# Kernel optimization log

Hardware: AMD Instinct MI355X
Metric: run time of the kernel (lower is better)

## Reference

```python
import jax, jax.numpy as jnp
import numpy as np

B, H, N, D, BD, K = 8, 8, 65536, 128, 64, 32


def _l2norm(x, eps=1e-12):
    n = jnp.linalg.norm(x, axis=-1, keepdims=True)
    return x / jnp.maximum(n, eps)


def _topk_sparse_softmax(sim, k):
    # softmax over the top-k entries per (b,h); zeros elsewhere (== masked_fill -inf softmax)
    vals, idx = jax.lax.top_k(sim, k)              # [B,H,k]
    wk = jax.nn.softmax(vals, axis=-1)
    b = jnp.arange(sim.shape[0])[:, None, None]
    h = jnp.arange(sim.shape[1])[None, :, None]
    return jnp.zeros_like(sim).at[b, h, idx].set(wk)  # [B,H,N]


def setup_inputs() -> dict:
    key = jax.random.key(0)
    ks = jax.random.split(key, 14)
    return {
        "memory": jax.random.normal(ks[0], (B, N, D), jnp.float32),
        "read_keys": jax.random.normal(ks[1], (B, H, D), jnp.float32),
        "write_keys": jax.random.normal(ks[2], (B, H, D), jnp.float32),
        "write_vals": jax.random.normal(ks[3], (B, H, D), jnp.float32),
        "erase": jax.random.uniform(ks[4], (B, H), jnp.float32),
        "add_gate": jax.random.uniform(ks[5], (B, H), jnp.float32),
        "beta_r": jax.random.uniform(ks[6], (B, H), jnp.float32),
        "beta_w": jax.random.uniform(ks[7], (B, H), jnp.float32),
        "W_b1": jax.random.normal(ks[8], (D, BD), jnp.float32) * 0.02,
        "b_b1": jnp.zeros((BD,), jnp.float32),
        "W_b2": jax.random.normal(ks[9], (BD, D), jnp.float32) * 0.02,
        "b_b2": jnp.zeros((D,), jnp.float32),
        "W_merge": jax.random.normal(ks[10], (H * D, D), jnp.float32) * 0.02,
        "b_merge": jnp.zeros((D,), jnp.float32),
        "ln_g": jnp.ones((D,), jnp.float32),
        "ln_b": jnp.zeros((D,), jnp.float32),
        "decay_gate": jnp.ones((N,), jnp.float32) * 0.99,
    }


def reference(memory, read_keys, write_keys, write_vals, erase, add_gate,
              beta_r, beta_w, W_b1, b_b1, W_b2, b_b2, W_merge, b_merge,
              ln_g, ln_b, decay_gate):
    # ---- write (erase/add with top-k addressing, head-mean, normalize, decay) ----
    cvals = jax.nn.gelu(write_vals @ W_b1 + b_b1, approximate=False) @ W_b2 + b_b2  # [B,H,D]
    sim_w = jnp.einsum('bhd,bnd->bhn', _l2norm(write_keys), _l2norm(memory)) * beta_w[..., None]
    ww = _topk_sparse_softmax(sim_w, K)                                # [B,H,N]
    # mean_h[mem*(1-w*e)] = mem*(1-mean_h(w*e));  mean_h[w*add*cvals] via einsum/H
    erase_mean = (ww * erase[..., None]).mean(axis=1)                  # [B,N]
    add_part = jnp.einsum('bhn,bhd->bnd', ww * add_gate[..., None], cvals) / H
    mem2 = memory * (1.0 - erase_mean)[..., None] + add_part
    mem2 = _l2norm(mem2 + 1e-8)
    mem2 = mem2 * jax.nn.sigmoid(decay_gate)[None, :, None]            # decay gate

    # ---- read (from updated memory) ----
    sim_r = jnp.einsum('bhd,bnd->bhn', _l2norm(read_keys), _l2norm(mem2)) * beta_r[..., None]
    wr = _topk_sparse_softmax(sim_r, K)
    rph = jnp.einsum('bhn,bnd->bhd', wr, mem2).reshape(mem2.shape[0], H * D)
    merged = rph @ W_merge + b_merge                                   # [B,D]
    mu = merged.mean(axis=-1, keepdims=True)
    var = jnp.mean((merged - mu) ** 2, axis=-1, keepdims=True)
    out = (merged - mu) / jnp.sqrt(var + 1e-5) * ln_g + ln_b           # LayerNorm
    return out
```

## Files before the change

kernel.cpp:

```cpp
#include <hip/hip_runtime.h>
#include <hip/hip_bf16.h>

#define BB   8
#define HH   8
#define NN   65536
#define DD   128
#define BDIM 64
#define KK   32


#define OFF_SIMW 0u
#define OFF_SIMR (OFF_SIMW + 4194304u)
#define OFF_NWK  (OFF_SIMR + 4194304u)
#define OFF_NRK  (OFF_NWK + 8192u)
#define OFF_CV   (OFF_NRK + 8192u)
#define OFF_WIDX (OFF_CV + 8192u)
#define OFF_WVAL (OFF_WIDX + 2048u)
#define OFF_RIDX (OFF_WVAL + 2048u)
#define OFF_RVAL (OFF_RIDX + 2048u)
#define OFF_M2U  (OFF_RVAL + 2048u)
#define OFF_RPH  (OFF_M2U + 262144u)

__device__ __forceinline__ float brsum128(float v, float* sred, int tid) {
  #pragma unroll
  for (int o = 32; o > 0; o >>= 1) v += __shfl_xor(v, o);
  __syncthreads();
  if ((tid & 63) == 0) sred[tid >> 6] = v;
  __syncthreads();
  return sred[0] + sred[1];
}

__global__ __launch_bounds__(128) void k1_setup(
    const float* __restrict__ wkeys, const float* __restrict__ rkeys,
    const float* __restrict__ wvals,
    const float* __restrict__ beta_r, const float* __restrict__ beta_w,
    const float* __restrict__ W_b1, const float* __restrict__ b_b1,
    const float* __restrict__ W_b2, const float* __restrict__ b_b2,
    float* __restrict__ nwk, float* __restrict__ nrk,
    float* __restrict__ cvals, float* __restrict__ rph) {
  int g = blockIdx.x;
  int d = threadIdx.x;
  __shared__ float sred[2];
  __shared__ float wv_s[DD];
  __shared__ float hid[BDIM];

  rph[g * DD + d] = 0.f;

  float wk = wkeys[g * DD + d];
  float rk = rkeys[g * DD + d];
  float wv = wvals[g * DD + d];
  wv_s[d] = wv;

  float s = brsum128(wk * wk, sred, d);
  nwk[g * DD + d] = wk / fmaxf(sqrtf(s), 1e-12f) * beta_w[g];
  s = brsum128(rk * rk, sred, d);
  nrk[g * DD + d] = rk / fmaxf(sqrtf(s), 1e-12f) * beta_r[g];

  __syncthreads();
  if (d < BDIM) {
    float a = b_b1[d];
    #pragma unroll 4
    for (int dd = 0; dd < DD; ++dd) a += wv_s[dd] * W_b1[dd * BDIM + d];
    hid[d] = a * 0.5f * (1.f + erff(a * 0.70710678118654752f));
  }
  __syncthreads();
  float c = b_b2[d];
  #pragma unroll 4
  for (int j = 0; j < BDIM; ++j) c += hid[j] * W_b2[j * DD + d];
  cvals[g * DD + d] = c;
}

__global__ __launch_bounds__(256) void k2_sims(
    const float* __restrict__ mem,
    const float* __restrict__ nwk, const float* __restrict__ nrk,
    float* __restrict__ simw, float* __restrict__ simr) {
  int blk = blockIdx.x;
  int b   = blk >> 8;
  int n   = ((blk & 255) << 8) + threadIdx.x;
  const float4* rowp = (const float4*)(mem + ((size_t)b * NN + n) * DD);

  float dw[HH] = {0,0,0,0,0,0,0,0};
  float dr[HH] = {0,0,0,0,0,0,0,0};
  float nw = 0.f, nr = 0.f;
  const float* kw = nwk + b * HH * DD;
  const float* kr = nrk + b * HH * DD;

  float4 q[8], p[8];
  #pragma unroll
  for (int i = 0; i < 8; ++i) q[i] = rowp[i];
  #pragma unroll
  for (int g = 0; g < 4; ++g) {
    if (g < 3) {
      #pragma unroll
      for (int i = 0; i < 8; ++i) p[i] = rowp[(g + 1) * 8 + i];
    }
    #pragma unroll
    for (int i = 0; i < 8; ++i) {
      float xs[4] = {q[i].x, q[i].y, q[i].z, q[i].w};
      #pragma unroll
      for (int e = 0; e < 4; ++e) {
        float xv = xs[e];
        float xr = xv + 1e-8f;
        nw += xv * xv;
        nr += xr * xr;
        int d = g * 32 + i * 4 + e;
        #pragma unroll
        for (int h = 0; h < HH; ++h) {
          dw[h] += xv * kw[h * DD + d];
          dr[h] += xr * kr[h * DD + d];
        }
      }
    }
    #pragma unroll
    for (int i = 0; i < 8; ++i) q[i] = p[i];
  }
  float riw = 1.f / fmaxf(sqrtf(nw), 1e-12f);
  float rir = 1.f / fmaxf(sqrtf(nr), 1e-12f);
  #pragma unroll
  for (int h = 0; h < HH; ++h) {
    simw[(size_t)(b * HH + h) * NN + n] = dw[h] * riw;
    simr[(size_t)(b * HH + h) * NN + n] = dr[h] * rir;
  }
}

#define NBKT 4096
#define MAXC 4096
#define SAMP 2048
__global__ __launch_bounds__(1024) void k_topk(
    const float* __restrict__ sims, int* __restrict__ oidx, float* __restrict__ oval) {
  int blk = blockIdx.x;
  int tid = threadIdx.x;
  const float4* s4 = (const float4*)(sims + (size_t)blk * NN);
  __shared__ unsigned hist[NBKT];
  __shared__ unsigned segsum[64];
  __shared__ float cv[MAXC];
  __shared__ int   ci[MAXC];
  __shared__ int   sthr, scnt;
  __shared__ float selv[KK];
  __shared__ int   seli[KK];

  #pragma unroll
  for (int i = tid; i < NBKT; i += 1024) hist[i] = 0u;
  if (tid == 0) scnt = 0;
  __syncthreads();

  #pragma unroll
  for (int i = tid; i < SAMP; i += 1024) {
    float4 v = s4[i];
    float xs[4] = {v.x, v.y, v.z, v.w};
    #pragma unroll
    for (int e = 0; e < 4; ++e) {
      unsigned u = __float_as_uint(xs[e]);
      u = (u & 0x80000000u) ? ~u : (u | 0x80000000u);
      atomicAdd(&hist[u >> 20], 1u);
    }
  }
  __syncthreads();

  if (tid < 64) {
    unsigned ssum = 0;
    int base = tid << 6;
    #pragma unroll
    for (int j = 0; j < 64; ++j) ssum += hist[base + ((j + tid) & 63)];
    segsum[tid] = ssum;
  }
  __syncthreads();
  if (tid == 0) {
    unsigned acc = 0;
    int sg = 63;
    while (sg > 0 && acc + segsum[sg] < KK) { acc += segsum[sg]; --sg; }
    int t = (sg << 6) + 63;
    while (t > (sg << 6) && acc + hist[t] < KK) { acc += hist[t]; --t; }
    sthr = t;
  }
  __syncthreads();

  int thr = sthr;
  #pragma unroll 2
  for (int i = tid; i < NN / 4; i += 1024) {
    float4 v = s4[i];
    float xs[4] = {v.x, v.y, v.z, v.w};
    #pragma unroll
    for (int e = 0; e < 4; ++e) {
      float vv = xs[e];
      unsigned u = __float_as_uint(vv);
      u = (u & 0x80000000u) ? ~u : (u | 0x80000000u);
      if ((int)(u >> 20) >= thr) {
        int p = atomicAdd(&scnt, 1);
        if (p < MAXC) { cv[p] = vv; ci[p] = i * 4 + e; }
      }
    }
  }
  __syncthreads();
  int nc = min(scnt, MAXC);

  if (tid < 64) {
    for (int k = 0; k < KK; ++k) {
      unsigned long long best = 0ull, lbest = 0ull;
      int lj = -1;
      for (int j = tid; j < nc; j += 64) {
        float v = cv[j];
        unsigned u = __float_as_uint(v);
        u = (u & 0x80000000u) ? ~u : (u | 0x80000000u);
        unsigned long long key = ((unsigned long long)u << 32) | (unsigned)(~(unsigned)ci[j]);
        if (key > lbest) { lbest = key; lj = j; }
      }
      best = lbest;
      #pragma unroll
      for (int o = 32; o > 0; o >>= 1) {
        unsigned long long t = __shfl_xor(best, o);
        if (t > best) best = t;
      }
      if (lbest == best && lj >= 0) cv[lj] = -1e30f;
      if (tid == 0) {
        unsigned u = (unsigned)(best >> 32);
        float v = (u & 0x80000000u) ? __uint_as_float(u & 0x7fffffffu) : __uint_as_float(~u);
        selv[k] = v;
        seli[k] = (int)~(unsigned)(best & 0xffffffffu);
      }
    }
    if (tid == 0) {
      float m0 = selv[0], ssum = 0.f;
      float es[KK];
      #pragma unroll
      for (int k = 0; k < KK; ++k) { es[k] = expf(selv[k] - m0); ssum += es[k]; }
      float inv = 1.f / ssum;
      #pragma unroll
      for (int k = 0; k < KK; ++k) {
        oidx[blk * KK + k] = seli[k];
        oval[blk * KK + k] = es[k] * inv;
      }
    }
  }
}

__global__ __launch_bounds__(128) void k4_write(
    const float* __restrict__ mem, const float* __restrict__ erase,
    const float* __restrict__ adg,
    const int* __restrict__ widx, const float* __restrict__ wval,
    const float* __restrict__ cvals, const float* __restrict__ nrk,
    float* __restrict__ mem2u, float* __restrict__ simr) {
  int b  = blockIdx.x >> 8;
  int sl = blockIdx.x & 255;
  int d  = threadIdx.x;
  __shared__ int   swi[256];
  __shared__ float swv[256];
  __shared__ float sred[2 * 9];

  swi[d]       = widx[b * 256 + d];
  swi[d + 128] = widx[b * 256 + d + 128];
  swv[d]       = wval[b * 256 + d];
  swv[d + 128] = wval[b * 256 + d + 128];
  __syncthreads();

  int n = swi[sl];
  for (int j = 0; j < sl; ++j) if (swi[j] == n) return;

  float E = 0.f, addd = 0.f;
  #pragma unroll
  for (int h = 0; h < HH; ++h) {
    float er = erase[b * HH + h];
    float ag = adg[b * HH + h];
    float aw = 0.f;
    #pragma unroll 4
    for (int k = 0; k < KK; ++k) {
      int j = h * KK + k;
      if (swi[j] == n) { float wv = swv[j]; E += wv * er; aw += wv; }
    }
    addd += aw * ag * cvals[(b * HH + h) * DD + d];
  }
  float mval = mem[((size_t)b * NN + n) * DD + d];
  float v = mval * (1.f - E * 0.125f) + addd * 0.125f + 1e-8f;

  float r[9];
  r[0] = v * v;
  #pragma unroll
  for (int h = 0; h < HH; ++h) r[1 + h] = nrk[(b * HH + h) * DD + d] * v;
  #pragma unroll
  for (int o = 32; o > 0; o >>= 1) {
    #pragma unroll
    for (int i = 0; i < 9; ++i) r[i] += __shfl_xor(r[i], o);
  }
  if ((d & 63) == 0) {
    int w = d >> 6;
    #pragma unroll
    for (int i = 0; i < 9; ++i) sred[w * 9 + i] = r[i];
  }
  __syncthreads();
  float S    = sred[0] + sred[9];
  float rinv = 1.f / fmaxf(sqrtf(S), 1e-12f);
  mem2u[(size_t)(b * 256 + sl) * DD + d] = v * rinv;
  if (d < HH) simr[(size_t)(b * HH + d) * NN + n] = (sred[1 + d] + sred[9 + 1 + d]) * rinv;
}

__global__ __launch_bounds__(128) void k6_gather(
    const float* __restrict__ mem, const float* __restrict__ decay,
    const int* __restrict__ widx, const int* __restrict__ ridx,
    const float* __restrict__ rval, const float* __restrict__ mem2u,
    float* __restrict__ rph) {
  int b   = blockIdx.x >> 8;
  int rem = blockIdx.x & 255;
  int d   = threadIdx.x;
  __shared__ int swi[256];
  __shared__ float sred[2];
  swi[d]       = widx[b * 256 + d];
  swi[d + 128] = widx[b * 256 + d + 128];
  __syncthreads();

  int n   = ridx[b * HH * KK + rem];
  float w = rval[b * HH * KK + rem];
  float sc = 1.f / (1.f + expf(-decay[n]));
  int slot = -1;
  for (int j = 0; j < 256; ++j) if (swi[j] == n) { slot = j; break; }
  float u;
  if (slot >= 0) {
    u = mem2u[(size_t)(b * 256 + slot) * DD + d];
  } else {
    float v = mem[((size_t)b * NN + n) * DD + d] + 1e-8f;
    float S = brsum128(v * v, sred, d);
    u = v / fmaxf(sqrtf(S), 1e-12f);
  }
  int h = rem >> 5;
  atomicAdd(&rph[(b * HH + h) * DD + d], w * sc * u);
}

__global__ __launch_bounds__(512) void k7_merge(
    const float* __restrict__ rph, const float* __restrict__ W_merge,
    const float* __restrict__ b_merge, const float* __restrict__ ln_g,
    const float* __restrict__ ln_b, float* __restrict__ out) {
  int b = blockIdx.x;
  int tid = threadIdx.x;
  int d = tid & 127;
  int p = tid >> 7;
  __shared__ float acc_s[4][DD];
  __shared__ float accf[DD];
  __shared__ float smu, svar;

  float a = 0.f;
  int j0 = p * 256;
  #pragma unroll 4
  for (int j = j0; j < j0 + 256; ++j)
    a += rph[b * HH * DD + j] * W_merge[j * DD + d];
  acc_s[p][d] = a;
  __syncthreads();
  if (tid < DD) accf[d] = b_merge[d] + acc_s[0][d] + acc_s[1][d] + acc_s[2][d] + acc_s[3][d];
  __syncthreads();
  if (tid < 64) {
    float x0 = accf[tid], x1 = accf[tid + 64];
    float s1 = x0 + x1, s2 = x0 * x0 + x1 * x1;
    #pragma unroll
    for (int o = 32; o > 0; o >>= 1) { s1 += __shfl_xor(s1, o); s2 += __shfl_xor(s2, o); }
    if (tid == 0) { smu = s1 * (1.f / DD); svar = s2 * (1.f / DD) - smu * smu; }
  }
  __syncthreads();
  if (tid < DD)
    out[b * DD + d] = (accf[d] - smu) * rsqrtf(svar + 1e-5f) * ln_g[d] + ln_b[d];
}

extern "C" void kernel_launch(void* const* d_in, const int* in_sizes, int n_in,
                              void* d_out, int out_size, void* d_ws, size_t ws_size,
                              hipStream_t stream) {
  const float* memory  = (const float*)d_in[0];
  const float* rkeys   = (const float*)d_in[1];
  const float* wkeys   = (const float*)d_in[2];
  const float* wvals   = (const float*)d_in[3];
  const float* erase   = (const float*)d_in[4];
  const float* adg     = (const float*)d_in[5];
  const float* beta_r  = (const float*)d_in[6];
  const float* beta_w  = (const float*)d_in[7];
  const float* W_b1    = (const float*)d_in[8];
  const float* b_b1    = (const float*)d_in[9];
  const float* W_b2    = (const float*)d_in[10];
  const float* b_b2    = (const float*)d_in[11];
  const float* W_merge = (const float*)d_in[12];
  const float* b_merge = (const float*)d_in[13];
  const float* ln_g    = (const float*)d_in[14];
  const float* ln_b    = (const float*)d_in[15];
  const float* decay   = (const float*)d_in[16];

  float* ws   = (float*)d_ws;
  float* simw = ws + OFF_SIMW;
  float* simr = ws + OFF_SIMR;
  float* nwk  = ws + OFF_NWK;
  float* nrk  = ws + OFF_NRK;
  float* cv   = ws + OFF_CV;
  int*   widx = (int*)(ws + OFF_WIDX);
  float* wval = ws + OFF_WVAL;
  int*   ridx = (int*)(ws + OFF_RIDX);
  float* rval = ws + OFF_RVAL;
  float* m2u  = ws + OFF_M2U;
  float* rph  = ws + OFF_RPH;

  hipLaunchKernelGGL(k1_setup, dim3(BB * HH), dim3(128), 0, stream,
                     wkeys, rkeys, wvals, beta_r, beta_w, W_b1, b_b1, W_b2, b_b2,
                     nwk, nrk, cv, rph);
  hipLaunchKernelGGL(k2_sims, dim3(BB * (NN / 256)), dim3(256), 0, stream,
                     memory, nwk, nrk, simw, simr);
  hipLaunchKernelGGL(k_topk, dim3(BB * HH), dim3(1024), 0, stream, simw, widx, wval);
  hipLaunchKernelGGL(k4_write, dim3(BB * 256), dim3(128), 0, stream,
                     memory, erase, adg, widx, wval, cv, nrk, m2u, simr);
  hipLaunchKernelGGL(k_topk, dim3(BB * HH), dim3(1024), 0, stream, simr, ridx, rval);
  hipLaunchKernelGGL(k6_gather, dim3(BB * 256), dim3(128), 0, stream,
                     memory, decay, widx, ridx, rval, m2u, rph);
  hipLaunchKernelGGL(k7_merge, dim3(BB), dim3(512), 0, stream,
                     rph, W_merge, b_merge, ln_g, ln_b, (float*)d_out);
}
```

Measured before the change: 599.7 us.

## Split top-k into per-chunk local selection and a merge kernel

Replaces the single 64-block top-k kernel with a two-stage scheme. Each of 16 chunks per (b,h) row builds its own full-chunk histogram, keeps its values in registers, and extracts a local top-32 into workspace. A one-wave merge kernel then picks the global top-32 from the 512 candidates and computes the softmax. This aims to use far more of the GPU's compute units than 64 blocks can, and it drops the second global read of the row, at the cost of an extra launch and a workspace round trip.

```diff
diff --git a/kernel.cpp b/kernel.cpp
--- a/kernel.cpp
+++ b/kernel.cpp
@@ -20,6 +20,8 @@
 #define OFF_RVAL (OFF_RIDX + 2048u)
 #define OFF_M2U  (OFF_RVAL + 2048u)
 #define OFF_RPH  (OFF_M2U + 262144u)
+#define OFF_CVA  (OFF_RPH + 8192u)
+#define OFF_CIA  (OFF_CVA + 32768u)
 
 __device__ __forceinline__ float brsum128(float v, float* sred, int tid) {
   #pragma unroll
@@ -28,6 +30,14 @@
   if ((tid & 63) == 0) sred[tid >> 6] = v;
   __syncthreads();
   return sred[0] + sred[1];
+}
+
+__device__ __forceinline__ unsigned ordf(float v) {
+  unsigned u = __float_as_uint(v);
+  return (u & 0x80000000u) ? ~u : (u | 0x80000000u);
+}
+__device__ __forceinline__ float unordf(unsigned u) {
+  return (u & 0x80000000u) ? __uint_as_float(u & 0x7fffffffu) : __uint_as_float(~u);
 }
 
 __global__ __launch_bounds__(128) void k1_setup(
@@ -123,35 +133,39 @@
   }
 }
 
-#define NBKT 4096
-#define MAXC 4096
-#define SAMP 2048
-__global__ __launch_bounds__(1024) void k_topk(
-    const float* __restrict__ sims, int* __restrict__ oidx, float* __restrict__ oval) {
+#define TKCH  16
+#define CHLEN (NN / TKCH)
+#define MAXCL 1024
+
+__global__ __launch_bounds__(256) void k_topk_local(
+    const float* __restrict__ sims, float* __restrict__ cval, int* __restrict__ cidx) {
   int blk = blockIdx.x;
+  int bh  = blk >> 4;
+  int ch  = blk & 15;
   int tid = threadIdx.x;
-  const float4* s4 = (const float4*)(sims + (size_t)blk * NN);
-  __shared__ unsigned hist[NBKT];
+  const float4* s4 = (const float4*)(sims + (size_t)bh * NN + ch * CHLEN);
+  __shared__ unsigned hist[4096];
   __shared__ unsigned segsum[64];
-  __shared__ float cv[MAXC];
-  __shared__ int   ci[MAXC];
+  __shared__ float cv[MAXCL];
+  __shared__ int   ci[MAXCL];
   __shared__ int   sthr, scnt;
-  __shared__ float selv[KK];
-  __shared__ int   seli[KK];
-
-  #pragma unroll
-  for (int i = tid; i < NBKT; i += 1024) hist[i] = 0u;
+
+  #pragma unroll
+  for (int i = tid; i < 4096; i += 256) hist[i] = 0u;
   if (tid == 0) scnt = 0;
   __syncthreads();
 
-  #pragma unroll
-  for (int i = tid; i < SAMP; i += 1024) {
-    float4 v = s4[i];
-    float xs[4] = {v.x, v.y, v.z, v.w};
+  float4 v[4];
+  #pragma unroll
+  for (int j = 0; j < 4; ++j) v[j] = s4[tid + j * 256];
+  unsigned ub[16];
+  #pragma unroll
+  for (int j = 0; j < 4; ++j) {
+    float xs[4] = {v[j].x, v[j].y, v[j].z, v[j].w};
     #pragma unroll
     for (int e = 0; e < 4; ++e) {
-      unsigned u = __float_as_uint(xs[e]);
-      u = (u & 0x80000000u) ? ~u : (u | 0x80000000u);
+      unsigned u = ordf(xs[e]);
+      ub[j * 4 + e] = u;
       atomicAdd(&hist[u >> 20], 1u);
     }
   }
@@ -176,36 +190,31 @@
   __syncthreads();
 
   int thr = sthr;
-  #pragma unroll 2
-  for (int i = tid; i < NN / 4; i += 1024) {
-    float4 v = s4[i];
-    float xs[4] = {v.x, v.y, v.z, v.w};
-    #pragma unroll
-    for (int e = 0; e < 4; ++e) {
-      float vv = xs[e];
-      unsigned u = __float_as_uint(vv);
-      u = (u & 0x80000000u) ? ~u : (u | 0x80000000u);
-      if ((int)(u >> 20) >= thr) {
-        int p = atomicAdd(&scnt, 1);
-        if (p < MAXC) { cv[p] = vv; ci[p] = i * 4 + e; }
+  #pragma unroll
+  for (int j = 0; j < 16; ++j) {
+    unsigned u = ub[j];
+    if ((int)(u >> 20) >= thr) {
+      int p = atomicAdd(&scnt, 1);
+      if (p < MAXCL) {
+        int li = (tid + (j >> 2) * 256) * 4 + (j & 3);
+        cv[p] = unordf(u);
+        ci[p] = ch * CHLEN + li;
       }
     }
   }
   __syncthreads();
-  int nc = min(scnt, MAXC);
+  int nc = min(scnt, MAXCL);
 
   if (tid < 64) {
     for (int k = 0; k < KK; ++k) {
-      unsigned long long best = 0ull, lbest = 0ull;
+      unsigned long long lbest = 0ull;
       int lj = -1;
       for (int j = tid; j < nc; j += 64) {
-        float v = cv[j];
-        unsigned u = __float_as_uint(v);
-        u = (u & 0x80000000u) ? ~u : (u | 0x80000000u);
-        unsigned long long key = ((unsigned long long)u << 32) | (unsigned)(~(unsigned)ci[j]);
+        unsigned long long key = ((unsigned long long)ordf(cv[j]) << 32) |
+                                 (unsigned)(~(unsigned)ci[j]);
         if (key > lbest) { lbest = key; lj = j; }
       }
-      best = lbest;
+      unsigned long long best = lbest;
       #pragma unroll
       for (int o = 32; o > 0; o >>= 1) {
         unsigned long long t = __shfl_xor(best, o);
@@ -213,23 +222,54 @@
       }
       if (lbest == best && lj >= 0) cv[lj] = -1e30f;
       if (tid == 0) {
-        unsigned u = (unsigned)(best >> 32);
-        float v = (u & 0x80000000u) ? __uint_as_float(u & 0x7fffffffu) : __uint_as_float(~u);
-        selv[k] = v;
-        seli[k] = (int)~(unsigned)(best & 0xffffffffu);
+        cval[blk * KK + k] = unordf((unsigned)(best >> 32));
+        cidx[blk * KK + k] = (int)~(unsigned)(best & 0xffffffffu);
       }
     }
-    if (tid == 0) {
-      float m0 = selv[0], ssum = 0.f;
-      float es[KK];
-      #pragma unroll
-      for (int k = 0; k < KK; ++k) { es[k] = expf(selv[k] - m0); ssum += es[k]; }
-      float inv = 1.f / ssum;
-      #pragma unroll
-      for (int k = 0; k < KK; ++k) {
-        oidx[blk * KK + k] = seli[k];
-        oval[blk * KK + k] = es[k] * inv;
-      }
+  }
+}
+
+__global__ __launch_bounds__(64) void k_topk_merge(
+    const float* __restrict__ cval, const int* __restrict__ cidx,
+    int* __restrict__ oidx, float* __restrict__ oval) {
+  int bh   = blockIdx.x;
+  int lane = threadIdx.x;
+  __shared__ float selv[KK];
+  __shared__ int   seli[KK];
+  unsigned long long key[8];
+  #pragma unroll
+  for (int j = 0; j < 8; ++j) {
+    int i = lane + j * 64;
+    float v  = cval[bh * (TKCH * KK) + i];
+    int   id = cidx[bh * (TKCH * KK) + i];
+    key[j] = ((unsigned long long)ordf(v) << 32) | (unsigned)(~(unsigned)id);
+  }
+  for (int k = 0; k < KK; ++k) {
+    unsigned long long best = 0ull;
+    #pragma unroll
+    for (int j = 0; j < 8; ++j) best = (key[j] > best) ? key[j] : best;
+    #pragma unroll
+    for (int o = 32; o > 0; o >>= 1) {
+      unsigned long long t = __shfl_xor(best, o);
+      if (t > best) best = t;
+    }
+    #pragma unroll
+    for (int j = 0; j < 8; ++j) key[j] = (key[j] == best) ? 0ull : key[j];
+    if (lane == 0) {
+      selv[k] = unordf((unsigned)(best >> 32));
+      seli[k] = (int)~(unsigned)(best & 0xffffffffu);
+    }
+  }
+  if (lane == 0) {
+    float m0 = selv[0], ssum = 0.f;
+    float es[KK];
+    #pragma unroll
+    for (int k = 0; k < KK; ++k) { es[k] = expf(selv[k] - m0); ssum += es[k]; }
+    float inv = 1.f / ssum;
+    #pragma unroll
+    for (int k = 0; k < KK; ++k) {
+      oidx[bh * KK + k] = seli[k];
+      oval[bh * KK + k] = es[k] * inv;
     }
   }
 }
@@ -390,16 +430,24 @@
   float* rval = ws + OFF_RVAL;
   float* m2u  = ws + OFF_M2U;
   float* rph  = ws + OFF_RPH;
+  float* cva  = ws + OFF_CVA;
+  int*   cia  = (int*)(ws + OFF_CIA);
 
   hipLaunchKernelGGL(k1_setup, dim3(BB * HH), dim3(128), 0, stream,
                      wkeys, rkeys, wvals, beta_r, beta_w, W_b1, b_b1, W_b2, b_b2,
                      nwk, nrk, cv, rph);
   hipLaunchKernelGGL(k2_sims, dim3(BB * (NN / 256)), dim3(256), 0, stream,
                      memory, nwk, nrk, simw, simr);
-  hipLaunchKernelGGL(k_topk, dim3(BB * HH), dim3(1024), 0, stream, simw, widx, wval);
+  hipLaunchKernelGGL(k_topk_local, dim3(BB * HH * TKCH), dim3(256), 0, stream,
+                     simw, cva, cia);
+  hipLaunchKernelGGL(k_topk_merge, dim3(BB * HH), dim3(64), 0, stream,
+                     cva, cia, widx, wval);
   hipLaunchKernelGGL(k4_write, dim3(BB * 256), dim3(128), 0, stream,
                      memory, erase, adg, widx, wval, cv, nrk, m2u, simr);
-  hipLaunchKernelGGL(k_topk, dim3(BB * HH), dim3(1024), 0, stream, simr, ridx, rval);
+  hipLaunchKernelGGL(k_topk_local, dim3(BB * HH * TKCH), dim3(256), 0, stream,
+                     simr, cva, cia);
+  hipLaunchKernelGGL(k_topk_merge, dim3(BB * HH), dim3(64), 0, stream,
+                     cva, cia, ridx, rval);
   hipLaunchKernelGGL(k6_gather, dim3(BB * 256), dim3(128), 0, stream,
                      memory, decay, widx, ridx, rval, m2u, rph);
   hipLaunchKernelGGL(k7_merge, dim3(BB), dim3(512), 0, stream,
```

Result: no change. 588.1 us (-1.9%).
